# Optimization experiments

Hardware: AMD Instinct MI355X
Metric: run time of the kernel (lower is better)

Reference implementation:

```python
import jax, jax.numpy as jnp
import numpy as np

S, B, D, E, C, FF = 2048, 4, 1024, 8, 2048, 4096
N = S * B


def setup_inputs() -> dict:
    key = jax.random.key(0)
    ks = jax.random.split(key, 7)
    return {
        "hidden_states": jax.random.normal(ks[0], (S, B, D), dtype=jnp.float32),
        "combine_weights": jax.random.uniform(ks[1], (N, E), dtype=jnp.float32),
        "top_idx": jax.random.randint(ks[2], (C, E), 0, N, dtype=jnp.int64),
        "W1": jax.random.normal(ks[3], (E, D, FF), dtype=jnp.float32) * (1.0 / np.sqrt(D)),
        "b1": jnp.zeros((E, FF), dtype=jnp.float32),
        "W2": jax.random.normal(ks[4], (E, FF, D), dtype=jnp.float32) * (1.0 / np.sqrt(FF)),
        "b2": jnp.zeros((E, D), dtype=jnp.float32),
    }


def reference(hidden_states, combine_weights, top_idx, W1, b1, W2, b2):
    # MoE dispatch -> per-expert MLP -> weighted scatter-add combine
    s, b, d = hidden_states.shape
    x = hidden_states.reshape(-1, d)                      # [N, D]
    tok = top_idx.T                                       # [E, C] token ids per expert
    gathered = x[tok]                                     # [E, C, D] dispatch gather
    h = jax.nn.gelu(jnp.einsum('ecd,edf->ecf', gathered, W1) + b1[:, None, :])
    out_e = jnp.einsum('ecf,efd->ecd', h, W2) + b2[:, None, :]  # [E, C, D]
    e_ids = jnp.arange(tok.shape[0])[:, None]             # [E, 1]
    w = combine_weights[tok, e_ids]                       # [E, C] per-token gate weight
    weighted = (out_e * w[..., None]).reshape(-1, d)      # [E*C, D]
    out = jnp.zeros_like(x).at[tok.reshape(-1)].add(weighted)  # scatter-add combine
    return out.reshape(s, b, d)
```

## Files before the change

### kernel.cpp

```cpp
#include <hip/hip_runtime.h>
#include <stdint.h>

#define S_DIM 2048
#define B_DIM 4
#define D_DIM 1024
#define E_DIM 8
#define C_DIM 2048
#define FF_DIM 4096
#define N_DIM (S_DIM * B_DIM)

typedef unsigned short u16;
using bf16x8 = __attribute__((ext_vector_type(8))) __bf16;
using u16x8  = __attribute__((ext_vector_type(8))) unsigned short;
using f32x4  = __attribute__((ext_vector_type(4))) float;

__device__ __forceinline__ u16 f2bf(float f) {
  uint32_t u = __float_as_uint(f);
  u += 0x7fffu + ((u >> 16) & 1u);
  return (u16)(u >> 16);
}
__device__ __forceinline__ float bf2f(u16 h) {
  return __uint_as_float(((uint32_t)h) << 16);
}
__device__ __forceinline__ void split2(float v, u16& hi, u16& lo) {
  hi = f2bf(v);
  lo = f2bf(v - bf2f(hi));
}
__device__ __forceinline__ float gelu_tanh(float x) {
  float u = 0.7978845608028654f * (x + 0.044715f * x * x * x);
  return 0.5f * x * (1.0f + tanhf(u));
}
__device__ __forceinline__ void cp16(const void* g, void* l) {
  __builtin_amdgcn_global_load_lds(
      (const __attribute__((address_space(1))) void*)g,
      (__attribute__((address_space(3))) void*)l,
      16, 0, 0);
}

__global__ __launch_bounds__(256) void detect_i64_kernel(
    const int* __restrict__ t, int* __restrict__ flag) {
  int i = blockIdx.x * 256 + threadIdx.x;
  if (i < (E_DIM * C_DIM) / 2 && t[2 * i + 1] != 0) atomicOr(flag, 1);
}

__global__ __launch_bounds__(256) void prep_tok_kernel(
    const void* __restrict__ top_idx, const float* __restrict__ cw,
    const int* __restrict__ flag, int* __restrict__ tok32, float* __restrict__ wg) {
  int t = blockIdx.x * 256 + threadIdx.x;
  if (t >= E_DIM * C_DIM) return;
  int e = t / C_DIM, c = t % C_DIM;
  int tid;
  if (*flag == 0) {
    tid = (int)((const long long*)top_idx)[(size_t)c * E_DIM + e];
  } else {
    tid = ((const int*)top_idx)[(size_t)c * E_DIM + e];
  }
  tid &= (N_DIM - 1);
  tok32[t] = tid;
  wg[t] = cw[(size_t)tid * E_DIM + e];
}

__global__ __launch_bounds__(256) void split_x_kernel(
    const float* __restrict__ x, u16* __restrict__ xh, u16* __restrict__ xl, int wlo) {
  size_t i = ((size_t)blockIdx.x * 256 + threadIdx.x) * 8;
  const float4* p = (const float4*)(x + i);
  float4 v0 = p[0], v1 = p[1];
  float vv[8] = {v0.x, v0.y, v0.z, v0.w, v1.x, v1.y, v1.z, v1.w};
  u16x8 hv, lv;
#pragma unroll
  for (int j = 0; j < 8; ++j) { u16 h, l; split2(vv[j], h, l); hv[j] = h; lv[j] = l; }
  *(u16x8*)(xh + i) = hv;
  if (wlo) *(u16x8*)(xl + i) = lv;
}

__global__ __launch_bounds__(256) void trans_split_kernel(
    const float* __restrict__ in, u16* __restrict__ ohi, u16* __restrict__ olo,
    int R, int Cc, int wlo) {
  __shared__ float T[64][65];
  const int e = blockIdx.z;
  const int c0 = blockIdx.x * 64, r0 = blockIdx.y * 64;
  const int tx = threadIdx.x & 63, ty = threadIdx.x >> 6;
  const float* ein = in + (size_t)e * R * Cc;
  u16* eh = ohi + (size_t)e * R * Cc;
  u16* elo = wlo ? (olo + (size_t)e * R * Cc) : nullptr;
#pragma unroll
  for (int i = 0; i < 16; ++i) {
    int r = ty + i * 4;
    T[r][tx] = ein[(size_t)(r0 + r) * Cc + (c0 + tx)];
  }
  __syncthreads();
  const int tr = (threadIdx.x & 7) * 8;
  const int cbase = threadIdx.x >> 3;
#pragma unroll
  for (int i = 0; i < 2; ++i) {
    const int c = cbase + i * 32;
    u16x8 hv, lv;
#pragma unroll
    for (int j = 0; j < 8; ++j) {
      u16 h, l; split2(T[tr + j][c], h, l);
      hv[j] = h; lv[j] = l;
    }
    const size_t o = (size_t)(c0 + c) * R + (r0 + tr);
    *(u16x8*)(eh + o) = hv;
    if (wlo) *(u16x8*)(elo + o) = lv;
  }
}

template <bool LOB>
__global__ __launch_bounds__(256) void gemm1_kernel(
    const u16* __restrict__ xs_hi, const u16* __restrict__ xs_lo,
    const u16* __restrict__ w1t_hi, const u16* __restrict__ w1t_lo,
    const int* __restrict__ tok32, const float* __restrict__ b1,
    u16* __restrict__ h_hi, u16* __restrict__ h_lo) {
  __shared__ u16 As_hi[4096], Bs_hi[4096];
  __shared__ u16 As_lo[LOB ? 4096 : 4], Bs_lo[LOB ? 4096 : 4];
  __shared__ int tok_s[128];

  const int e = blockIdx.z, cb = blockIdx.y, fb = blockIdx.x;
  const int t = threadIdx.x, lane = t & 63, w = t >> 6;
  const int wm = w >> 1, wn = w & 1;

  if (t < 128) tok_s[t] = tok32[e * C_DIM + cb * 128 + t];
  __syncthreads();

  const u16 *sAh[2], *sAl[2], *sBh[2], *sBl[2];
#pragma unroll
  for (int i = 0; i < 2; ++i) {
    const int q = i * 256 + t, row = q >> 2, sub = q & 3;
    const size_t arow = (size_t)tok_s[row] * D_DIM + sub * 8;
    sAh[i] = xs_hi + arow;
    if constexpr (LOB) sAl[i] = xs_lo + arow;
    const size_t brow = ((size_t)(e * FF_DIM + fb * 128 + row)) * D_DIM + sub * 8;
    sBh[i] = w1t_hi + brow;
    if constexpr (LOB) sBl[i] = w1t_lo + brow;
  }

  int aOff[4], bOff[4];
#pragma unroll
  for (int mi = 0; mi < 4; ++mi)
    aOff[mi] = (wm * 64 + mi * 16 + (lane & 15)) * 32 + (lane >> 4) * 8;
#pragma unroll
  for (int ni = 0; ni < 4; ++ni)
    bOff[ni] = (wn * 64 + ni * 16 + (lane & 15)) * 32 + (lane >> 4) * 8;

  f32x4 zero = {0.f, 0.f, 0.f, 0.f};
  f32x4 acc[4][4];
#pragma unroll
  for (int mi = 0; mi < 4; ++mi)
#pragma unroll
    for (int ni = 0; ni < 4; ++ni) acc[mi][ni] = zero;

  const int wbase = w * 64 * 8;

  for (int kk = 0; kk < D_DIM / 32; ++kk) {
    const int ke = kk * 32;
#pragma unroll
    for (int i = 0; i < 2; ++i) {
      const int lofs = i * 2048 + wbase;
      cp16(sAh[i] + ke, &As_hi[lofs]);
      cp16(sBh[i] + ke, &Bs_hi[lofs]);
      if constexpr (LOB) {
        cp16(sAl[i] + ke, &As_lo[lofs]);
        cp16(sBl[i] + ke, &Bs_lo[lofs]);
      }
    }
    __syncthreads();

    bf16x8 ah[4], bh[4], al[4], bl[4];
#pragma unroll
    for (int mi = 0; mi < 4; ++mi) {
      ah[mi] = *(const bf16x8*)&As_hi[aOff[mi]];
      if constexpr (LOB) al[mi] = *(const bf16x8*)&As_lo[aOff[mi]];
    }
#pragma unroll
    for (int ni = 0; ni < 4; ++ni) {
      bh[ni] = *(const bf16x8*)&Bs_hi[bOff[ni]];
      if constexpr (LOB) bl[ni] = *(const bf16x8*)&Bs_lo[bOff[ni]];
    }
#pragma unroll
    for (int mi = 0; mi < 4; ++mi)
#pragma unroll
      for (int ni = 0; ni < 4; ++ni) {
        acc[mi][ni] = __builtin_amdgcn_mfma_f32_16x16x32_bf16(ah[mi], bh[ni], acc[mi][ni], 0, 0, 0);
        if constexpr (LOB) {
          acc[mi][ni] = __builtin_amdgcn_mfma_f32_16x16x32_bf16(ah[mi], bl[ni], acc[mi][ni], 0, 0, 0);
          acc[mi][ni] = __builtin_amdgcn_mfma_f32_16x16x32_bf16(al[mi], bh[ni], acc[mi][ni], 0, 0, 0);
        }
      }
    __syncthreads();
  }

  const int c_base0 = cb * 128 + wm * 64;
  const int f_base0 = fb * 128 + wn * 64;
#pragma unroll
  for (int ni = 0; ni < 4; ++ni) {
    const int f = f_base0 + ni * 16 + (lane & 15);
    const float bias = b1[e * FF_DIM + f];
#pragma unroll
    for (int mi = 0; mi < 4; ++mi) {
#pragma unroll
      for (int j = 0; j < 4; ++j) {
        const int c = c_base0 + mi * 16 + (lane >> 4) * 4 + j;
        float g = gelu_tanh(acc[mi][ni][j] + bias);
        u16 hh, ll; split2(g, hh, ll);
        const size_t off = ((size_t)(e * C_DIM + c)) * FF_DIM + f;
        h_hi[off] = hh;
        if constexpr (LOB) h_lo[off] = ll;
      }
    }
  }
}

template <bool LOB>
__global__ __launch_bounds__(256) void gemm2_kernel(
    const u16* __restrict__ h_hi, const u16* __restrict__ h_lo,
    const u16* __restrict__ w2t_hi, const u16* __restrict__ w2t_lo,
    const int* __restrict__ tok32, const float* __restrict__ wg,
    const float* __restrict__ b2, float* __restrict__ out) {
  __shared__ u16 As_hi[4096], Bs_hi[4096];
  __shared__ u16 As_lo[LOB ? 4096 : 4], Bs_lo[LOB ? 4096 : 4];
  __shared__ int tok_s[128];
  __shared__ float w_s[128];

  const int e = blockIdx.z, cb = blockIdx.y, db = blockIdx.x;
  const int t = threadIdx.x, lane = t & 63, w = t >> 6;
  const int wm = w >> 1, wn = w & 1;

  if (t < 128) {
    tok_s[t] = tok32[e * C_DIM + cb * 128 + t];
    w_s[t] = wg[e * C_DIM + cb * 128 + t];
  }

  const u16 *sAh[2], *sAl[2], *sBh[2], *sBl[2];
#pragma unroll
  for (int i = 0; i < 2; ++i) {
    const int q = i * 256 + t, row = q >> 2, sub = q & 3;
    const size_t arow = ((size_t)(e * C_DIM + cb * 128 + row)) * FF_DIM + sub * 8;
    sAh[i] = h_hi + arow;
    if constexpr (LOB) sAl[i] = h_lo + arow;
    const size_t brow = ((size_t)(e * D_DIM + db * 128 + row)) * FF_DIM + sub * 8;
    sBh[i] = w2t_hi + brow;
    if constexpr (LOB) sBl[i] = w2t_lo + brow;
  }

  int aOff[4], bOff[4];
#pragma unroll
  for (int mi = 0; mi < 4; ++mi)
    aOff[mi] = (wm * 64 + mi * 16 + (lane & 15)) * 32 + (lane >> 4) * 8;
#pragma unroll
  for (int ni = 0; ni < 4; ++ni)
    bOff[ni] = (wn * 64 + ni * 16 + (lane & 15)) * 32 + (lane >> 4) * 8;

  f32x4 zero = {0.f, 0.f, 0.f, 0.f};
  f32x4 acc[4][4];
#pragma unroll
  for (int mi = 0; mi < 4; ++mi)
#pragma unroll
    for (int ni = 0; ni < 4; ++ni) acc[mi][ni] = zero;

  const int wbase = w * 64 * 8;

  for (int kk = 0; kk < FF_DIM / 32; ++kk) {
    const int ke = kk * 32;
#pragma unroll
    for (int i = 0; i < 2; ++i) {
      const int lofs = i * 2048 + wbase;
      cp16(sAh[i] + ke, &As_hi[lofs]);
      cp16(sBh[i] + ke, &Bs_hi[lofs]);
      if constexpr (LOB) {
        cp16(sAl[i] + ke, &As_lo[lofs]);
        cp16(sBl[i] + ke, &Bs_lo[lofs]);
      }
    }
    __syncthreads();

    bf16x8 ah[4], bh[4], al[4], bl[4];
#pragma unroll
    for (int mi = 0; mi < 4; ++mi) {
      ah[mi] = *(const bf16x8*)&As_hi[aOff[mi]];
      if constexpr (LOB) al[mi] = *(const bf16x8*)&As_lo[aOff[mi]];
    }
#pragma unroll
    for (int ni = 0; ni < 4; ++ni) {
      bh[ni] = *(const bf16x8*)&Bs_hi[bOff[ni]];
      if constexpr (LOB) bl[ni] = *(const bf16x8*)&Bs_lo[bOff[ni]];
    }
#pragma unroll
    for (int mi = 0; mi < 4; ++mi)
#pragma unroll
      for (int ni = 0; ni < 4; ++ni) {
        acc[mi][ni] = __builtin_amdgcn_mfma_f32_16x16x32_bf16(ah[mi], bh[ni], acc[mi][ni], 0, 0, 0);
        if constexpr (LOB) {
          acc[mi][ni] = __builtin_amdgcn_mfma_f32_16x16x32_bf16(ah[mi], bl[ni], acc[mi][ni], 0, 0, 0);
          acc[mi][ni] = __builtin_amdgcn_mfma_f32_16x16x32_bf16(al[mi], bh[ni], acc[mi][ni], 0, 0, 0);
        }
      }
    __syncthreads();
  }

  const int dbase = db * 128 + wn * 64;
#pragma unroll
  for (int ni = 0; ni < 4; ++ni) {
    const int d = dbase + ni * 16 + (lane & 15);
    const float bias = b2[e * D_DIM + d];
#pragma unroll
    for (int mi = 0; mi < 4; ++mi) {
#pragma unroll
      for (int j = 0; j < 4; ++j) {
        const int cl = wm * 64 + mi * 16 + (lane >> 4) * 4 + j;
        const float val = (acc[mi][ni][j] + bias) * w_s[cl];
        atomicAdd(out + (size_t)tok_s[cl] * D_DIM + d, val);
      }
    }
  }
}

extern "C" void kernel_launch(void* const* d_in, const int* in_sizes, int n_in,
                              void* d_out, int out_size, void* d_ws, size_t ws_size,
                              hipStream_t stream) {
  (void)in_sizes; (void)n_in; (void)out_size;
  const float* x  = (const float*)d_in[0];
  const float* cw = (const float*)d_in[1];
  const void* tidx = d_in[2];
  const float* W1 = (const float*)d_in[3];
  const float* b1 = (const float*)d_in[4];
  const float* W2 = (const float*)d_in[5];
  const float* b2 = (const float*)d_in[6];
  float* out = (float*)d_out;

  const size_t nx  = (size_t)N_DIM * D_DIM;
  const size_t nw  = (size_t)E_DIM * FF_DIM * D_DIM;
  const size_t nh  = (size_t)E_DIM * C_DIM * FF_DIM;
  const size_t nEC = (size_t)E_DIM * C_DIM;

  const size_t need_hi   = (nx + 2 * nw + nh) * 2 + nEC * 8 + 64;
  const size_t need_full = (nx + 2 * nw + nh) * 4 + nEC * 8 + 64;

  const bool lo = ws_size >= need_full;
  if (!lo && ws_size < need_hi) return;

  char* p = (char*)d_ws;
  auto take = [&](size_t bytes) { char* r = p; p += bytes; return r; };
  u16* xs_hi  = (u16*)take(nx * 2);
  u16* xs_lo  = lo ? (u16*)take(nx * 2) : nullptr;
  u16* w1t_hi = (u16*)take(nw * 2);
  u16* w1t_lo = lo ? (u16*)take(nw * 2) : nullptr;
  u16* w2t_hi = (u16*)take(nw * 2);
  u16* w2t_lo = lo ? (u16*)take(nw * 2) : nullptr;
  u16* h_hi   = (u16*)take(nh * 2);
  u16* h_lo   = lo ? (u16*)take(nh * 2) : nullptr;
  int*  tok32 = (int*)take(nEC * 4);
  float* wg   = (float*)take(nEC * 4);
  int*  flag  = (int*)take(64);

  hipMemsetAsync(d_out, 0, nx * sizeof(float), stream);
  hipMemsetAsync(flag, 0, sizeof(int), stream);
  detect_i64_kernel<<<(int)((nEC / 2 + 255) / 256), 256, 0, stream>>>((const int*)tidx, flag);
  prep_tok_kernel<<<(int)((nEC + 255) / 256), 256, 0, stream>>>(tidx, cw, flag, tok32, wg);
  split_x_kernel<<<(int)(nx / 8 / 256), 256, 0, stream>>>(x, xs_hi, xs_lo, lo ? 1 : 0);
  trans_split_kernel<<<dim3(FF_DIM / 64, D_DIM / 64, E_DIM), 256, 0, stream>>>(
      W1, w1t_hi, w1t_lo, D_DIM, FF_DIM, lo ? 1 : 0);
  trans_split_kernel<<<dim3(D_DIM / 64, FF_DIM / 64, E_DIM), 256, 0, stream>>>(
      W2, w2t_hi, w2t_lo, FF_DIM, D_DIM, lo ? 1 : 0);

  const dim3 g1(FF_DIM / 128, C_DIM / 128, E_DIM);
  const dim3 g2(D_DIM / 128, C_DIM / 128, E_DIM);
  if (lo) {
    gemm1_kernel<true><<<g1, 256, 0, stream>>>(xs_hi, xs_lo, w1t_hi, w1t_lo, tok32, b1, h_hi, h_lo);
    gemm2_kernel<true><<<g2, 256, 0, stream>>>(h_hi, h_lo, w2t_hi, w2t_lo, tok32, wg, b2, out);
  } else {
    gemm1_kernel<false><<<g1, 256, 0, stream>>>(xs_hi, nullptr, w1t_hi, nullptr, tok32, b1, h_hi, nullptr);
    gemm2_kernel<false><<<g2, 256, 0, stream>>>(h_hi, nullptr, w2t_hi, nullptr, tok32, wg, b2, out);
  }
}
```

Baseline: 855.8 us.

## Drop bf16 hi/lo split, double-buffer LDS tiles, and remap blocks across XCDs

Removes the three-term bf16 split (hi/lo compensation) path so every tensor is converted to a single bf16 and each GEMM step issues one MFMA instead of three. The GEMM main loops now double-buffer LDS, prefetching the next K tile while computing on the current one. Block indices are remapped linearly with a stride of 8 so neighbouring tiles land on the same XCD. The cost is reduced accuracy, since products now use plain bf16 inputs rather than the compensated split, and this may exceed tolerance.

Result: no change. 857.7 us (+0.2%).

```diff
diff --git a/kernel.cpp b/kernel.cpp
--- a/kernel.cpp
+++ b/kernel.cpp
@@ -18,13 +18,6 @@
   uint32_t u = __float_as_uint(f);
   u += 0x7fffu + ((u >> 16) & 1u);
   return (u16)(u >> 16);
-}
-__device__ __forceinline__ float bf2f(u16 h) {
-  return __uint_as_float(((uint32_t)h) << 16);
-}
-__device__ __forceinline__ void split2(float v, u16& hi, u16& lo) {
-  hi = f2bf(v);
-  lo = f2bf(v - bf2f(hi));
 }
 __device__ __forceinline__ float gelu_tanh(float x) {
   float u = 0.7978845608028654f * (x + 0.044715f * x * x * x);
@@ -61,28 +54,25 @@
 }
 
 __global__ __launch_bounds__(256) void split_x_kernel(
-    const float* __restrict__ x, u16* __restrict__ xh, u16* __restrict__ xl, int wlo) {
+    const float* __restrict__ x, u16* __restrict__ xh) {
   size_t i = ((size_t)blockIdx.x * 256 + threadIdx.x) * 8;
   const float4* p = (const float4*)(x + i);
   float4 v0 = p[0], v1 = p[1];
   float vv[8] = {v0.x, v0.y, v0.z, v0.w, v1.x, v1.y, v1.z, v1.w};
-  u16x8 hv, lv;
-#pragma unroll
-  for (int j = 0; j < 8; ++j) { u16 h, l; split2(vv[j], h, l); hv[j] = h; lv[j] = l; }
+  u16x8 hv;
+#pragma unroll
+  for (int j = 0; j < 8; ++j) hv[j] = f2bf(vv[j]);
   *(u16x8*)(xh + i) = hv;
-  if (wlo) *(u16x8*)(xl + i) = lv;
 }
 
 __global__ __launch_bounds__(256) void trans_split_kernel(
-    const float* __restrict__ in, u16* __restrict__ ohi, u16* __restrict__ olo,
-    int R, int Cc, int wlo) {
+    const float* __restrict__ in, u16* __restrict__ ohi, int R, int Cc) {
   __shared__ float T[64][65];
   const int e = blockIdx.z;
   const int c0 = blockIdx.x * 64, r0 = blockIdx.y * 64;
   const int tx = threadIdx.x & 63, ty = threadIdx.x >> 6;
   const float* ein = in + (size_t)e * R * Cc;
   u16* eh = ohi + (size_t)e * R * Cc;
-  u16* elo = wlo ? (olo + (size_t)e * R * Cc) : nullptr;
 #pragma unroll
   for (int i = 0; i < 16; ++i) {
     int r = ty + i * 4;
@@ -94,45 +84,39 @@
 #pragma unroll
   for (int i = 0; i < 2; ++i) {
     const int c = cbase + i * 32;
-    u16x8 hv, lv;
-#pragma unroll
-    for (int j = 0; j < 8; ++j) {
-      u16 h, l; split2(T[tr + j][c], h, l);
-      hv[j] = h; lv[j] = l;
-    }
-    const size_t o = (size_t)(c0 + c) * R + (r0 + tr);
-    *(u16x8*)(eh + o) = hv;
-    if (wlo) *(u16x8*)(elo + o) = lv;
-  }
-}
-
-template <bool LOB>
+    u16x8 hv;
+#pragma unroll
+    for (int j = 0; j < 8; ++j) hv[j] = f2bf(T[tr + j][c]);
+    *(u16x8*)(eh + (size_t)(c0 + c) * R + (r0 + tr)) = hv;
+  }
+}
+
 __global__ __launch_bounds__(256) void gemm1_kernel(
-    const u16* __restrict__ xs_hi, const u16* __restrict__ xs_lo,
-    const u16* __restrict__ w1t_hi, const u16* __restrict__ w1t_lo,
+    const u16* __restrict__ xs, const u16* __restrict__ w1t,
     const int* __restrict__ tok32, const float* __restrict__ b1,
-    u16* __restrict__ h_hi, u16* __restrict__ h_lo) {
-  __shared__ u16 As_hi[4096], Bs_hi[4096];
-  __shared__ u16 As_lo[LOB ? 4096 : 4], Bs_lo[LOB ? 4096 : 4];
+    u16* __restrict__ h) {
+  __shared__ u16 As[2][4096], Bs[2][4096];
   __shared__ int tok_s[128];
 
-  const int e = blockIdx.z, cb = blockIdx.y, fb = blockIdx.x;
+  const int GX = FF_DIM / 128, GY = C_DIM / 128;
+  const int nblk = GX * GY * E_DIM;
+  const int lin = ((int)blockIdx.x & 7) * (nblk / 8) + ((int)blockIdx.x >> 3);
+  const int fb = lin % GX;
+  const int cb = (lin / GX) % GY;
+  const int e  = lin / (GX * GY);
+
   const int t = threadIdx.x, lane = t & 63, w = t >> 6;
   const int wm = w >> 1, wn = w & 1;
 
   if (t < 128) tok_s[t] = tok32[e * C_DIM + cb * 128 + t];
   __syncthreads();
 
-  const u16 *sAh[2], *sAl[2], *sBh[2], *sBl[2];
+  const u16 *sA[2], *sB[2];
 #pragma unroll
   for (int i = 0; i < 2; ++i) {
     const int q = i * 256 + t, row = q >> 2, sub = q & 3;
-    const size_t arow = (size_t)tok_s[row] * D_DIM + sub * 8;
-    sAh[i] = xs_hi + arow;
-    if constexpr (LOB) sAl[i] = xs_lo + arow;
-    const size_t brow = ((size_t)(e * FF_DIM + fb * 128 + row)) * D_DIM + sub * 8;
-    sBh[i] = w1t_hi + brow;
-    if constexpr (LOB) sBl[i] = w1t_lo + brow;
+    sA[i] = xs + (size_t)tok_s[row] * D_DIM + sub * 8;
+    sB[i] = w1t + ((size_t)(e * FF_DIM + fb * 128 + row)) * D_DIM + sub * 8;
   }
 
   int aOff[4], bOff[4];
@@ -152,41 +136,34 @@
 
   const int wbase = w * 64 * 8;
 
-  for (int kk = 0; kk < D_DIM / 32; ++kk) {
-    const int ke = kk * 32;
-#pragma unroll
-    for (int i = 0; i < 2; ++i) {
-      const int lofs = i * 2048 + wbase;
-      cp16(sAh[i] + ke, &As_hi[lofs]);
-      cp16(sBh[i] + ke, &Bs_hi[lofs]);
-      if constexpr (LOB) {
-        cp16(sAl[i] + ke, &As_lo[lofs]);
-        cp16(sBl[i] + ke, &Bs_lo[lofs]);
+#pragma unroll
+  for (int i = 0; i < 2; ++i) {
+    cp16(sA[i], &As[0][i * 2048 + wbase]);
+    cp16(sB[i], &Bs[0][i * 2048 + wbase]);
+  }
+  __syncthreads();
+
+  const int NT = D_DIM / 32;
+  for (int kk = 0; kk < NT; ++kk) {
+    const int cur = kk & 1;
+    if (kk + 1 < NT) {
+      const int ke = (kk + 1) * 32, nxt = cur ^ 1;
+#pragma unroll
+      for (int i = 0; i < 2; ++i) {
+        cp16(sA[i] + ke, &As[nxt][i * 2048 + wbase]);
+        cp16(sB[i] + ke, &Bs[nxt][i * 2048 + wbase]);
       }
     }
-    __syncthreads();
-
-    bf16x8 ah[4], bh[4], al[4], bl[4];
-#pragma unroll
-    for (int mi = 0; mi < 4; ++mi) {
-      ah[mi] = *(const bf16x8*)&As_hi[aOff[mi]];
-      if constexpr (LOB) al[mi] = *(const bf16x8*)&As_lo[aOff[mi]];
-    }
-#pragma unroll
-    for (int ni = 0; ni < 4; ++ni) {
-      bh[ni] = *(const bf16x8*)&Bs_hi[bOff[ni]];
-      if constexpr (LOB) bl[ni] = *(const bf16x8*)&Bs_lo[bOff[ni]];
-    }
+    bf16x8 af[4], bf[4];
+#pragma unroll
+    for (int mi = 0; mi < 4; ++mi) af[mi] = *(const bf16x8*)&As[cur][aOff[mi]];
+#pragma unroll
+    for (int ni = 0; ni < 4; ++ni) bf[ni] = *(const bf16x8*)&Bs[cur][bOff[ni]];
 #pragma unroll
     for (int mi = 0; mi < 4; ++mi)
 #pragma unroll
-      for (int ni = 0; ni < 4; ++ni) {
-        acc[mi][ni] = __builtin_amdgcn_mfma_f32_16x16x32_bf16(ah[mi], bh[ni], acc[mi][ni], 0, 0, 0);
-        if constexpr (LOB) {
-          acc[mi][ni] = __builtin_amdgcn_mfma_f32_16x16x32_bf16(ah[mi], bl[ni], acc[mi][ni], 0, 0, 0);
-          acc[mi][ni] = __builtin_amdgcn_mfma_f32_16x16x32_bf16(al[mi], bh[ni], acc[mi][ni], 0, 0, 0);
-        }
-      }
+      for (int ni = 0; ni < 4; ++ni)
+        acc[mi][ni] = __builtin_amdgcn_mfma_f32_16x16x32_bf16(af[mi], bf[ni], acc[mi][ni], 0, 0, 0);
     __syncthreads();
   }
 
@@ -201,28 +178,27 @@
 #pragma unroll
       for (int j = 0; j < 4; ++j) {
         const int c = c_base0 + mi * 16 + (lane >> 4) * 4 + j;
-        float g = gelu_tanh(acc[mi][ni][j] + bias);
-        u16 hh, ll; split2(g, hh, ll);
-        const size_t off = ((size_t)(e * C_DIM + c)) * FF_DIM + f;
-        h_hi[off] = hh;
-        if constexpr (LOB) h_lo[off] = ll;
+        h[((size_t)(e * C_DIM + c)) * FF_DIM + f] = f2bf(gelu_tanh(acc[mi][ni][j] + bias));
       }
     }
   }
 }
 
-template <bool LOB>
 __global__ __launch_bounds__(256) void gemm2_kernel(
-    const u16* __restrict__ h_hi, const u16* __restrict__ h_lo,
-    const u16* __restrict__ w2t_hi, const u16* __restrict__ w2t_lo,
+    const u16* __restrict__ h, const u16* __restrict__ w2t,
     const int* __restrict__ tok32, const float* __restrict__ wg,
     const float* __restrict__ b2, float* __restrict__ out) {
-  __shared__ u16 As_hi[4096], Bs_hi[4096];
-  __shared__ u16 As_lo[LOB ? 4096 : 4], Bs_lo[LOB ? 4096 : 4];
+  __shared__ u16 As[2][4096], Bs[2][4096];
   __shared__ int tok_s[128];
   __shared__ float w_s[128];
 
-  const int e = blockIdx.z, cb = blockIdx.y, db = blockIdx.x;
+  const int GX = D_DIM / 128, GY = C_DIM / 128;
+  const int nblk = GX * GY * E_DIM;
+  const int lin = ((int)blockIdx.x & 7) * (nblk / 8) + ((int)blockIdx.x >> 3);
+  const int db = lin % GX;
+  const int cb = (lin / GX) % GY;
+  const int e  = lin / (GX * GY);
+
   const int t = threadIdx.x, lane = t & 63, w = t >> 6;
   const int wm = w >> 1, wn = w & 1;
 
@@ -231,16 +207,12 @@
     w_s[t] = wg[e * C_DIM + cb * 128 + t];
   }
 
-  const u16 *sAh[2], *sAl[2], *sBh[2], *sBl[2];
+  const u16 *sA[2], *sB[2];
 #pragma unroll
   for (int i = 0; i < 2; ++i) {
     const int q = i * 256 + t, row = q >> 2, sub = q & 3;
-    const size_t arow = ((size_t)(e * C_DIM + cb * 128 + row)) * FF_DIM + sub * 8;
-    sAh[i] = h_hi + arow;
-    if constexpr (LOB) sAl[i] = h_lo + arow;
-    const size_t brow = ((size_t)(e * D_DIM + db * 128 + row)) * FF_DIM + sub * 8;
-    sBh[i] = w2t_hi + brow;
-    if constexpr (LOB) sBl[i] = w2t_lo + brow;
+    sA[i] = h + ((size_t)(e * C_DIM + cb * 128 + row)) * FF_DIM + sub * 8;
+    sB[i] = w2t + ((size_t)(e * D_DIM + db * 128 + row)) * FF_DIM + sub * 8;
   }
 
   int aOff[4], bOff[4];
@@ -260,41 +232,35 @@
 
   const int wbase = w * 64 * 8;
 
-  for (int kk = 0; kk < FF_DIM / 32; ++kk) {
-    const int ke = kk * 32;
-#pragma unroll
-    for (int i = 0; i < 2; ++i) {
-      const int lofs = i * 2048 + wbase;
-      cp16(sAh[i] + ke, &As_hi[lofs]);
-      cp16(sBh[i] + ke, &Bs_hi[lofs]);
-      if constexpr (LOB) {
-        cp16(sAl[i] + ke, &As_lo[lofs]);
-        cp16(sBl[i] + ke, &Bs_lo[lofs]);
+  __syncthreads();
+#pragma unroll
+  for (int i = 0; i < 2; ++i) {
+    cp16(sA[i], &As[0][i * 2048 + wbase]);
+    cp16(sB[i], &Bs[0][i * 2048 + wbase]);
+  }
+  __syncthreads();
+
+  const int NT = FF_DIM / 32;
+  for (int kk = 0; kk < NT; ++kk) {
+    const int cur = kk & 1;
+    if (kk + 1 < NT) {
+      const int ke = (kk + 1) * 32, nxt = cur ^ 1;
+#pragma unroll
+      for (int i = 0; i < 2; ++i) {
+        cp16(sA[i] + ke, &As[nxt][i * 2048 + wbase]);
+        cp16(sB[i] + ke, &Bs[nxt][i * 2048 + wbase]);
       }
     }
-    __syncthreads();
-
-    bf16x8 ah[4], bh[4], al[4], bl[4];
-#pragma unroll
-    for (int mi = 0; mi < 4; ++mi) {
-      ah[mi] = *(const bf16x8*)&As_hi[aOff[mi]];
-      if constexpr (LOB) al[mi] = *(const bf16x8*)&As_lo[aOff[mi]];
-    }
-#pragma unroll
-    for (int ni = 0; ni < 4; ++ni) {
-      bh[ni] = *(const bf16x8*)&Bs_hi[bOff[ni]];
-      if constexpr (LOB) bl[ni] = *(const bf16x8*)&Bs_lo[bOff[ni]];
-    }
+    bf16x8 af[4], bf[4];
+#pragma unroll
+    for (int mi = 0; mi < 4; ++mi) af[mi] = *(const bf16x8*)&As[cur][aOff[mi]];
+#pragma unroll
+    for (int ni = 0; ni < 4; ++ni) bf[ni] = *(const bf16x8*)&Bs[cur][bOff[ni]];
 #pragma unroll
     for (int mi = 0; mi < 4; ++mi)
 #pragma unroll
-      for (int ni = 0; ni < 4; ++ni) {
-        acc[mi][ni] = __builtin_amdgcn_mfma_f32_16x16x32_bf16(ah[mi], bh[ni], acc[mi][ni], 0, 0, 0);
-        if constexpr (LOB) {
-          acc[mi][ni] = __builtin_amdgcn_mfma_f32_16x16x32_bf16(ah[mi], bl[ni], acc[mi][ni], 0, 0, 0);
-          acc[mi][ni] = __builtin_amdgcn_mfma_f32_16x16x32_bf16(al[mi], bh[ni], acc[mi][ni], 0, 0, 0);
-        }
-      }
+      for (int ni = 0; ni < 4; ++ni)
+        acc[mi][ni] = __builtin_amdgcn_mfma_f32_16x16x32_bf16(af[mi], bf[ni], acc[mi][ni], 0, 0, 0);
     __syncthreads();
   }
 
@@ -333,43 +299,31 @@
   const size_t nh  = (size_t)E_DIM * C_DIM * FF_DIM;
   const size_t nEC = (size_t)E_DIM * C_DIM;
 
-  const size_t need_hi   = (nx + 2 * nw + nh) * 2 + nEC * 8 + 64;
-  const size_t need_full = (nx + 2 * nw + nh) * 4 + nEC * 8 + 64;
-
-  const bool lo = ws_size >= need_full;
-  if (!lo && ws_size < need_hi) return;
+  const size_t need = (nx + 2 * nw + nh) * 2 + nEC * 8 + 64;
+  if (ws_size < need) return;
 
   char* p = (char*)d_ws;
   auto take = [&](size_t bytes) { char* r = p; p += bytes; return r; };
-  u16* xs_hi  = (u16*)take(nx * 2);
-  u16* xs_lo  = lo ? (u16*)take(nx * 2) : nullptr;
-  u16* w1t_hi = (u16*)take(nw * 2);
-  u16* w1t_lo = lo ? (u16*)take(nw * 2) : nullptr;
-  u16* w2t_hi = (u16*)take(nw * 2);
-  u16* w2t_lo = lo ? (u16*)take(nw * 2) : nullptr;
-  u16* h_hi   = (u16*)take(nh * 2);
-  u16* h_lo   = lo ? (u16*)take(nh * 2) : nullptr;
+  u16* xs   = (u16*)take(nx * 2);
+  u16* w1t  = (u16*)take(nw * 2);
+  u16* w2t  = (u16*)take(nw * 2);
+  u16* hbuf = (u16*)take(nh * 2);
   int*  tok32 = (int*)take(nEC * 4);
-  float* wg   = (float*)take(nEC * 4);
+  float* wgp  = (float*)take(nEC * 4);
   int*  flag  = (int*)take(64);
 
   hipMemsetAsync(d_out, 0, nx * sizeof(float), stream);
   hipMemsetAsync(flag, 0, sizeof(int), stream);
   detect_i64_kernel<<<(int)((nEC / 2 + 255) / 256), 256, 0, stream>>>((const int*)tidx, flag);
-  prep_tok_kernel<<<(int)((nEC + 255) / 256), 256, 0, stream>>>(tidx, cw, flag, tok32, wg);
-  split_x_kernel<<<(int)(nx / 8 / 256), 256, 0, stream>>>(x, xs_hi, xs_lo, lo ? 1 : 0);
+  prep_tok_kernel<<<(int)((nEC + 255) / 256), 256, 0, stream>>>(tidx, cw, flag, tok32, wgp);
+  split_x_kernel<<<(int)(nx / 8 / 256), 256, 0, stream>>>(x, xs);
   trans_split_kernel<<<dim3(FF_DIM / 64, D_DIM / 64, E_DIM), 256, 0, stream>>>(
-      W1, w1t_hi, w1t_lo, D_DIM, FF_DIM, lo ? 1 : 0);
+      W1, w1t, D_DIM, FF_DIM);
   trans_split_kernel<<<dim3(D_DIM / 64, FF_DIM / 64, E_DIM), 256, 0, stream>>>(
-      W2, w2t_hi, w2t_lo, FF_DIM, D_DIM, lo ? 1 : 0);
-
-  const dim3 g1(FF_DIM / 128, C_DIM / 128, E_DIM);
-  const dim3 g2(D_DIM / 128, C_DIM / 128, E_DIM);
-  if (lo) {
-    gemm1_kernel<true><<<g1, 256, 0, stream>>>(xs_hi, xs_lo, w1t_hi, w1t_lo, tok32, b1, h_hi, h_lo);
-    gemm2_kernel<true><<<g2, 256, 0, stream>>>(h_hi, h_lo, w2t_hi, w2t_lo, tok32, wg, b2, out);
-  } else {
-    gemm1_kernel<false><<<g1, 256, 0, stream>>>(xs_hi, nullptr, w1t_hi, nullptr, tok32, b1, h_hi, nullptr);
-    gemm2_kernel<false><<<g2, 256, 0, stream>>>(h_hi, nullptr, w2t_hi, nullptr, tok32, wg, b2, out);
-  }
-}
+      W2, w2t, FF_DIM, D_DIM);
+
+  gemm1_kernel<<<(FF_DIM / 128) * (C_DIM / 128) * E_DIM, 256, 0, stream>>>(
+      xs, w1t, tok32, b1, hbuf);
+  gemm2_kernel<<<(D_DIM / 128) * (C_DIM / 128) * E_DIM, 256, 0, stream>>>(
+      hbuf, w2t, tok32, wgp, b2, out);
+}
```
